# Performance work log

Measured on AMD Instinct MI355X. Metric: run time of the kernel, lower is better.

Reference implementation:

```python
import jax, jax.numpy as jnp
import numpy as np

D_MODEL = 1024
NUM_HEADS = 16
HEAD_DIM = D_MODEL // NUM_HEADS


def setup_inputs() -> dict:
    key = jax.random.key(0)
    ks = jax.random.split(key, 12)
    B, S, D = 4, 2048, D_MODEL
    s = 1.0 / np.sqrt(D)
    return {
        "query": jax.random.normal(ks[0], (B, S, D), jnp.float32),
        "key": jax.random.normal(ks[1], (B, S, D), jnp.float32),
        "value": jax.random.normal(ks[2], (B, S, D), jnp.float32),
        "Wq": jax.random.normal(ks[3], (D, D), jnp.float32) * s,
        "bq": jax.random.normal(ks[4], (D,), jnp.float32) * 0.02,
        "Wk": jax.random.normal(ks[5], (D, D), jnp.float32) * s,
        "bk": jax.random.normal(ks[6], (D,), jnp.float32) * 0.02,
        "Wv": jax.random.normal(ks[7], (D, D), jnp.float32) * s,
        "bv": jax.random.normal(ks[8], (D,), jnp.float32) * 0.02,
        "Wo": jax.random.normal(ks[9], (D, D), jnp.float32) * s,
        "bo": jax.random.normal(ks[10], (D,), jnp.float32) * 0.02,
    }


def _split_heads(x):
    B, S, D = x.shape
    return x.reshape(B, S, NUM_HEADS, HEAD_DIM).transpose(0, 2, 1, 3)  # [B,H,S,hd]


def reference(query, key, value, Wq, bq, Wk, bk, Wv, bv, Wo, bo):
    q = _split_heads(query @ Wq + bq)
    k = _split_heads(key @ Wk + bk)
    v = _split_heads(value @ Wv + bv)
    # NOTE: original scales by 1/sqrt(d_model), not 1/sqrt(head_dim)
    scale = 1.0 / np.sqrt(D_MODEL).astype(np.float32)
    scores = jnp.einsum('bhqd,bhkd->bhqk', q, k) * scale  # [B,H,S,S]
    attn = jax.nn.softmax(scores, axis=-1)
    out = jnp.einsum('bhqk,bhkd->bhqd', attn, v)  # [B,H,S,hd]
    B, H, S, hd = out.shape
    out = out.transpose(0, 2, 1, 3).reshape(B, S, D_MODEL)
    out = out @ Wo + bo
    return out, attn
```

## Files before the change

### kernel.cpp

```cpp
#include <hip/hip_runtime.h>
#include <hip/hip_bf16.h>

typedef __bf16 bf16;
typedef __bf16 bf16x8 __attribute__((ext_vector_type(8)));
typedef __bf16 bf16x4 __attribute__((ext_vector_type(4)));
typedef __bf16 bf16x2 __attribute__((ext_vector_type(2)));
typedef float  f32x4  __attribute__((ext_vector_type(4)));
typedef float  f32x16 __attribute__((ext_vector_type(16)));
typedef unsigned int u32;

#define MFMA(A, B, C)   __builtin_amdgcn_mfma_f32_16x16x32_bf16((A), (B), (C), 0, 0, 0)
#define MFMA32(A, B, C) __builtin_amdgcn_mfma_f32_32x32x16_bf16((A), (B), (C), 0, 0, 0)

static constexpr int BATCH = 4, S = 2048, D = 1024, NH = 16, HD = 64;
static constexpr int M = BATCH * S;
static constexpr float KL = 0.045084220027780106f;

__device__ __forceinline__ void gload16(const void* g, void* l) {
  __builtin_amdgcn_global_load_lds(
      (const __attribute__((address_space(1))) void*)g,
      (__attribute__((address_space(3))) void*)l, 16, 0, 0);
}

__device__ __forceinline__ float fexp2(float x) {
#if __has_builtin(__builtin_amdgcn_exp2f)
  return __builtin_amdgcn_exp2f(x);
#else
  return exp2f(x);
#endif
}

__device__ __forceinline__ u32 pack2(float a, float b) {
  union { bf16x2 h; u32 u; } c;
  c.h = (bf16x2){(bf16)a, (bf16)b};
  return c.u;
}

union U4 { u32 w[4]; bf16x8 v; };

#define WAITV_BAR(n)                                        \
  asm volatile("s_waitcnt vmcnt(" #n ")" ::: "memory");     \
  __builtin_amdgcn_s_barrier();                             \
  __builtin_amdgcn_sched_barrier(0);

__global__ __launch_bounds__(256) void wt_convert(
    const float* __restrict__ W0, const float* __restrict__ W1,
    const float* __restrict__ W2, const float* __restrict__ W3,
    bf16* __restrict__ WtAll)
{
  const float* W = blockIdx.y == 0 ? W0 : blockIdx.y == 1 ? W1
                 : blockIdx.y == 2 ? W2 : W3;
  bf16* dst = WtAll + (size_t)blockIdx.y * (D * D);
  int k0 = (blockIdx.x >> 4) * 64, n0 = (blockIdx.x & 15) * 64;
  __shared__ __align__(16) bf16 T[64][72];
  int tid = threadIdx.x;
#pragma unroll
  for (int i = 0; i < 4; ++i) {
    int c = tid + i * 256, r = c >> 4, seg = c & 15;
    float4 v = *reinterpret_cast<const float4*>(W + (size_t)(k0 + r) * D + n0 + seg * 4);
    T[seg * 4 + 0][r] = (bf16)v.x; T[seg * 4 + 1][r] = (bf16)v.y;
    T[seg * 4 + 2][r] = (bf16)v.z; T[seg * 4 + 3][r] = (bf16)v.w;
  }
  __syncthreads();
#pragma unroll
  for (int i = 0; i < 2; ++i) {
    int c = tid + i * 256, r = c >> 3, seg = c & 7;
    *reinterpret_cast<bf16x8*>(dst + (size_t)(n0 + r) * D + k0 + seg * 8) =
        *reinterpret_cast<const bf16x8*>(&T[r][seg * 8]);
  }
}

__global__ __launch_bounds__(256) void x_convert(
    const float* __restrict__ X0, const float* __restrict__ X1,
    const float* __restrict__ X2, bf16* __restrict__ Y)
{
  int t = blockIdx.y;
  const float* X = t == 0 ? X0 : t == 1 ? X1 : X2;
  bf16* Yp = Y + (size_t)t * M * D;
  int idx = blockIdx.x * 256 + threadIdx.x;
#pragma unroll
  for (int i = 0; i < 4; ++i) {
    size_t j = (size_t)idx + (size_t)i * 524288;
    float4 v = reinterpret_cast<const float4*>(X)[j];
    bf16x4 o; o[0] = (bf16)v.x; o[1] = (bf16)v.y; o[2] = (bf16)v.z; o[3] = (bf16)v.w;
    reinterpret_cast<bf16x4*>(Yp)[j] = o;
  }
}

__global__ __launch_bounds__(256) void qkv_gemm(
    const bf16* __restrict__ Xb, const bf16* __restrict__ WtAll,
    const float* __restrict__ bq, const float* __restrict__ bk, const float* __restrict__ bv,
    bf16* __restrict__ Qb, bf16* __restrict__ Kb, bf16* __restrict__ Vtb)
{
  int v = blockIdx.y;
  const bf16*  X    = Xb + (size_t)v * M * D;
  const bf16*  Wt   = WtAll + (size_t)v * (D * D);
  const float* bias = v == 0 ? bq : v == 1 ? bk : bv;

  int x = blockIdx.x;
  int swz = (x & 7) * 64 + (x >> 3);
  int mt = swz >> 3, nt = swz & 7;
  int m0 = mt * 128, n0 = nt * 128;
  int tid = threadIdx.x, lane = tid & 63, w = tid >> 6;
  int wm = (w >> 1) * 64, wn = (w & 1) * 64;
  int lr = lane & 15, lg = lane >> 4;

  __shared__ __align__(16) unsigned char smem[34816];
  auto As = reinterpret_cast<bf16(*)[128][32]>(smem);
  auto Bs = reinterpret_cast<bf16(*)[128][32]>(smem + 16384);

  f32x4 acc[4][4] = {};

  int srow = w * 32 + (lane >> 2);
  int scol = (lane & 3) * 8;

  auto stage = [&](int buf, int ks) {
    const bf16* ga = X + (size_t)(m0 + srow) * D + ks * 32 + scol;
    bf16* la = &As[buf][w * 32][0];
    gload16(ga, la);
    gload16(ga + 16 * D, la + 16 * 32);
    const bf16* gb = Wt + (size_t)(n0 + srow) * D + ks * 32 + scol;
    bf16* lb = &Bs[buf][w * 32][0];
    gload16(gb, lb);
    gload16(gb + 16 * D, lb + 16 * 32);
  };

  stage(0, 0);
  for (int ks = 0; ks < 32; ++ks) {
    __syncthreads();
    if (ks < 31) stage((ks + 1) & 1, ks + 1);
    int buf = ks & 1;
    bf16x8 af[4], bfr[4];
#pragma unroll
    for (int i = 0; i < 4; ++i)
      af[i] = *reinterpret_cast<const bf16x8*>(&As[buf][wm + i * 16 + lr][8 * lg]);
#pragma unroll
    for (int j = 0; j < 4; ++j)
      bfr[j] = *reinterpret_cast<const bf16x8*>(&Bs[buf][wn + j * 16 + lr][8 * lg]);
#pragma unroll
    for (int i = 0; i < 4; ++i)
#pragma unroll
      for (int j = 0; j < 4; ++j)
        acc[i][j] = MFMA(af[i], bfr[j], acc[i][j]);
  }
  __syncthreads();

  if (v < 2) {
    bf16* Out = v == 0 ? Qb : Kb;
    float qs = v == 0 ? KL : 1.0f;
    auto Es = reinterpret_cast<bf16(*)[128]>(smem);
#pragma unroll
    for (int i = 0; i < 4; ++i)
#pragma unroll
      for (int j = 0; j < 4; ++j) {
        int n = wn + j * 16 + lr;
        float bias_n = bias[n0 + n];
#pragma unroll
        for (int r = 0; r < 4; ++r)
          Es[wm + i * 16 + 4 * lg + r][n] = (bf16)((acc[i][j][r] + bias_n) * qs);
      }
    __syncthreads();
#pragma unroll
    for (int i = 0; i < 8; ++i) {
      int c = tid + i * 256, r = c >> 4, seg = c & 15;
      int mg = m0 + r, b = mg >> 11, s = mg & 2047;
      int ng = n0 + seg * 8, h = ng >> 6, d = ng & 63;
      *reinterpret_cast<bf16x8*>(Out + (((size_t)(b * NH + h)) * S + s) * HD + d) =
          *reinterpret_cast<const bf16x8*>(&Es[r][seg * 8]);
    }
  } else {
    auto Es = reinterpret_cast<bf16(*)[136]>(smem);
#pragma unroll
    for (int i = 0; i < 4; ++i)
#pragma unroll
      for (int j = 0; j < 4; ++j) {
        int n = wn + j * 16 + lr;
        float bias_n = bias[n0 + n];
        bf16x4 t;
#pragma unroll
        for (int r = 0; r < 4; ++r) t[r] = (bf16)(acc[i][j][r] + bias_n);
        *reinterpret_cast<bf16x4*>(&Es[n][wm + i * 16 + 4 * lg]) = t;
      }
    __syncthreads();
#pragma unroll
    for (int i = 0; i < 8; ++i) {
      int c = tid + i * 256, r = c >> 4, seg = c & 15;
      int ng = n0 + r, h = ng >> 6, d = ng & 63;
      int mg = m0 + seg * 8, b = mg >> 11, s = mg & 2047;
      *reinterpret_cast<bf16x8*>(Vtb + (((size_t)(b * NH + h)) * HD + d) * S + s) =
          *reinterpret_cast<const bf16x8*>(&Es[r][seg * 8]);
    }
  }
}

__global__ __launch_bounds__(256) void attn_kernel(
    const bf16* __restrict__ Qb, const bf16* __restrict__ Kb, const bf16* __restrict__ Vtb,
    float* __restrict__ attn_out, bf16* __restrict__ ctx)
{
  int xx = blockIdx.x;
  int xcd = xx & 7, r8 = xx >> 3;
  int bh = xcd + 8 * (r8 >> 5);
  int qb = r8 & 31;
  int tid = threadIdx.x, lane = tid & 63, w = tid >> 6;
  int q32 = lane & 31, hi = lane >> 5;
  int qh = w & 1, kh = w >> 1;

  __shared__ __align__(16) bf16 Ks[2][64][64];
  __shared__ __align__(16) bf16 Vs[2][64][64];
  __shared__ __align__(16) float Ps[64][68];
  __shared__ float sums[2][64];

  int q_row = qb * 64 + qh * 32 + q32;
  const bf16* Qrow = Qb + ((size_t)bh * S + q_row) * HD;
  bf16x8 qreg[4];
#pragma unroll
  for (int c = 0; c < 4; ++c)
    qreg[c] = *reinterpret_cast<const bf16x8*>(Qrow + c * 16 + 8 * hi);

  auto stageK = [&](int buf, int kc) {
    const bf16* base = Kb + ((size_t)bh * S + kc * 64) * HD;
#pragma unroll
    for (int i = 0; i < 2; ++i) {
      int c = i * 256 + tid, row = c >> 3, j = c & 7;
      gload16(base + row * HD + 8 * (j ^ (row & 7)),
              reinterpret_cast<bf16*>(&Ks[buf][0][0]) + c * 8);
    }
  };
  auto stageV = [&](int buf, int kc) {
    const bf16* base = Vtb + (size_t)bh * HD * S + kc * 64;
#pragma unroll
    for (int i = 0; i < 2; ++i) {
      int c = i * 256 + tid, row = c >> 3, j = c & 7;
      gload16(base + (size_t)row * S + 8 * (j ^ (row & 7)),
              reinterpret_cast<bf16*>(&Vs[buf][0][0]) + c * 8);
    }
  };

  int krow = kh * 32 + q32, ks7 = krow & 7;

  float lrun = 0.f;
  stageK(0, 0);
  for (int kc = 0; kc < 32; ++kc) {
    if (kc < 31) {
      stageK((kc + 1) & 1, kc + 1);
      WAITV_BAR(2)
    } else {
      WAITV_BAR(0)
    }
    int buf = kc & 1;
    f32x16 sa = {};
#pragma unroll
    for (int c = 0; c < 4; ++c) {
      bf16x8 kf = *reinterpret_cast<const bf16x8*>(&Ks[buf][krow][8 * ((2 * c + hi) ^ ks7)]);
      sa = MFMA32(kf, qreg[c], sa);
    }
#pragma unroll
    for (int r = 0; r < 16; ++r) lrun += fexp2(sa[r]);
    __builtin_amdgcn_s_barrier();
  }
  lrun += __shfl_xor(lrun, 32);
  if (hi == 0) sums[kh][qh * 32 + q32] = lrun;
  __syncthreads();
  float lg2l = __log2f(sums[0][qh * 32 + q32] + sums[1][qh * 32 + q32]);

  f32x16 oaccA = {}, oaccB = {};
  float* ablk = attn_out + ((size_t)bh * S + qb * 64) * S;

  auto computeB = [&](int buf) {
    f32x16 sa = {};
#pragma unroll
    for (int c = 0; c < 4; ++c) {
      bf16x8 kf = *reinterpret_cast<const bf16x8*>(&Ks[buf][krow][8 * ((2 * c + hi) ^ ks7)]);
      sa = MFMA32(kf, qreg[c], sa);
    }
    u32 pku[8];
#pragma unroll
    for (int rq = 0; rq < 4; ++rq) {
      f32x4 pv;
#pragma unroll
      for (int j = 0; j < 4; ++j) pv[j] = fexp2(sa[rq * 4 + j] - lg2l);
      *reinterpret_cast<f32x4*>(&Ps[qh * 32 + q32][kh * 32 + 8 * rq + 4 * hi]) = pv;
      pku[rq * 2 + 0] = pack2(pv[0], pv[1]);
      pku[rq * 2 + 1] = pack2(pv[2], pv[3]);
    }
#pragma unroll
    for (int c2 = 0; c2 < 2; ++c2) {
      u32 myw0 = hi ? pku[4 * c2 + 2] : pku[4 * c2 + 0];
      u32 myw1 = hi ? pku[4 * c2 + 3] : pku[4 * c2 + 1];
      u32 sdw0 = hi ? pku[4 * c2 + 0] : pku[4 * c2 + 2];
      u32 sdw1 = hi ? pku[4 * c2 + 1] : pku[4 * c2 + 3];
      u32 r0 = __shfl_xor(sdw0, 32);
      u32 r1 = __shfl_xor(sdw1, 32);
      U4 f;
      f.w[0] = hi ? r0 : myw0;
      f.w[1] = hi ? r1 : myw1;
      f.w[2] = hi ? myw0 : r0;
      f.w[3] = hi ? myw1 : r1;
      {
        int vrow = q32, vs7 = vrow & 7;
        bf16x8 vf = *reinterpret_cast<const bf16x8*>(
            &Vs[buf][vrow][8 * ((4 * kh + 2 * c2 + hi) ^ vs7)]);
        oaccA = MFMA32(f.v, vf, oaccA);
      }
      {
        int vrow = 32 + q32, vs7 = vrow & 7;
        bf16x8 vf = *reinterpret_cast<const bf16x8*>(
            &Vs[buf][vrow][8 * ((4 * kh + 2 * c2 + hi) ^ vs7)]);
        oaccB = MFMA32(f.v, vf, oaccB);
      }
    }
  };

  int prow = tid >> 2, pc0 = (tid & 3) * 4;
  auto storeP = [&](int kc) {
    float* dst = ablk + (size_t)prow * S + kc * 64 + pc0;
#pragma unroll
    for (int i = 0; i < 4; ++i)
      __builtin_nontemporal_store(
          *reinterpret_cast<const f32x4*>(&Ps[prow][pc0 + 16 * i]),
          reinterpret_cast<f32x4*>(dst + 16 * i));
  };

  stageK(0, 0); stageV(0, 0);
  stageK(1, 1); stageV(1, 1);
  WAITV_BAR(4)
  computeB(0);
  __builtin_amdgcn_s_barrier();
  storeP(0);

  for (int kc = 1; kc < 32; ++kc) {
    if (kc < 31) {
      stageK((kc + 1) & 1, kc + 1);
      stageV((kc + 1) & 1, kc + 1);
      WAITV_BAR(8)
    } else {
      WAITV_BAR(4)
    }
    computeB(kc & 1);
    __builtin_amdgcn_s_barrier();
    storeP(kc);
  }

  float* fbuf = reinterpret_cast<float*>(&Ks[0][0][0]);
  if (kh == 1) {
#pragma unroll
    for (int reg = 0; reg < 16; ++reg) {
      int qloc = (reg & 3) + 8 * (reg >> 2) + 4 * hi;
      fbuf[(qh * 32 + qloc) * 64 + q32]      = oaccA[reg];
      fbuf[(qh * 32 + qloc) * 64 + 32 + q32] = oaccB[reg];
    }
  }
  __syncthreads();
  bf16* cs = reinterpret_cast<bf16*>(&Vs[0][0][0]);
  if (kh == 0) {
#pragma unroll
    for (int reg = 0; reg < 16; ++reg) {
      int qloc = (reg & 3) + 8 * (reg >> 2) + 4 * hi;
      cs[(qh * 32 + qloc) * 72 + q32] =
          (bf16)(oaccA[reg] + fbuf[(qh * 32 + qloc) * 64 + q32]);
      cs[(qh * 32 + qloc) * 72 + 32 + q32] =
          (bf16)(oaccB[reg] + fbuf[(qh * 32 + qloc) * 64 + 32 + q32]);
    }
  }
  __syncthreads();
  {
    int b = bh >> 4, h = bh & 15;
    int row = tid >> 2, cseg = (tid & 3) * 16;
    bf16* cp = ctx + ((size_t)b * S + qb * 64 + row) * D + h * HD + cseg;
    *reinterpret_cast<bf16x8*>(cp) =
        *reinterpret_cast<const bf16x8*>(&cs[row * 72 + cseg]);
    *reinterpret_cast<bf16x8*>(cp + 8) =
        *reinterpret_cast<const bf16x8*>(&cs[row * 72 + cseg + 8]);
  }
}

__global__ __launch_bounds__(256) void out_gemm(
    const bf16* __restrict__ ctx, const bf16* __restrict__ Wto,
    const float* __restrict__ bo, float* __restrict__ Out)
{
  int x = blockIdx.x;
  int swz = (x & 7) * 64 + (x >> 3);
  int mt = swz >> 3, nt = swz & 7;
  int m0 = mt * 128, n0 = nt * 128;
  int tid = threadIdx.x, lane = tid & 63, w = tid >> 6;
  int wm = (w >> 1) * 64, wn = (w & 1) * 64;
  int lr = lane & 15, lg = lane >> 4;

  __shared__ __align__(16) bf16 As[2][128][32];
  __shared__ __align__(16) bf16 Bs[2][128][32];

  f32x4 acc[4][4] = {};

  int srow = w * 32 + (lane >> 2);
  int scol = (lane & 3) * 8;

  auto stage = [&](int buf, int ks) {
    const bf16* ga = ctx + (size_t)(m0 + srow) * D + ks * 32 + scol;
    bf16* la = &As[buf][w * 32][0];
    gload16(ga, la);
    gload16(ga + 16 * D, la + 16 * 32);
    const bf16* gb = Wto + (size_t)(n0 + srow) * D + ks * 32 + scol;
    bf16* lb = &Bs[buf][w * 32][0];
    gload16(gb, lb);
    gload16(gb + 16 * D, lb + 16 * 32);
  };

  stage(0, 0);
  for (int ks = 0; ks < 32; ++ks) {
    __syncthreads();
    if (ks < 31) stage((ks + 1) & 1, ks + 1);
    int buf = ks & 1;
    bf16x8 af[4], bfr[4];
#pragma unroll
    for (int i = 0; i < 4; ++i)
      af[i] = *reinterpret_cast<const bf16x8*>(&As[buf][wm + i * 16 + lr][8 * lg]);
#pragma unroll
    for (int j = 0; j < 4; ++j)
      bfr[j] = *reinterpret_cast<const bf16x8*>(&Bs[buf][wn + j * 16 + lr][8 * lg]);
#pragma unroll
    for (int i = 0; i < 4; ++i)
#pragma unroll
      for (int j = 0; j < 4; ++j)
        acc[i][j] = MFMA(af[i], bfr[j], acc[i][j]);
  }

#pragma unroll
  for (int i = 0; i < 4; ++i)
#pragma unroll
    for (int j = 0; j < 4; ++j) {
      int n = n0 + wn + j * 16 + lr;
      float bias_n = bo[n];
#pragma unroll
      for (int r = 0; r < 4; ++r)
        Out[(size_t)(m0 + wm + i * 16 + 4 * lg + r) * D + n] = acc[i][j][r] + bias_n;
    }
}

extern "C" void kernel_launch(void* const* d_in, const int* in_sizes, int n_in,
                              void* d_out, int out_size, void* d_ws, size_t ws_size,
                              hipStream_t stream)
{
  const float* query = (const float*)d_in[0];
  const float* key   = (const float*)d_in[1];
  const float* value = (const float*)d_in[2];
  const float* Wq = (const float*)d_in[3]; const float* bq = (const float*)d_in[4];
  const float* Wk = (const float*)d_in[5]; const float* bk = (const float*)d_in[6];
  const float* Wv = (const float*)d_in[7]; const float* bv = (const float*)d_in[8];
  const float* Wo = (const float*)d_in[9]; const float* bo = (const float*)d_in[10];

  float* out  = (float*)d_out;
  float* attn = out + (size_t)M * D;

  char* ws = (char*)d_ws;
  const size_t MiB = 1048576;
  bf16* WtAll = (bf16*)ws;
  bf16* Xb    = (bf16*)(ws + 8 * MiB);
  bf16* Qb    = (bf16*)(ws + 56 * MiB);
  bf16* Kb    = (bf16*)(ws + 72 * MiB);
  bf16* Vtb   = (bf16*)(ws + 88 * MiB);
  bf16* ctx   = Xb;

  wt_convert<<<dim3(256, 4), 256, 0, stream>>>(Wq, Wk, Wv, Wo, WtAll);
  x_convert<<<dim3(2048, 3), 256, 0, stream>>>(query, key, value, Xb);
  qkv_gemm<<<dim3(512, 3), 256, 0, stream>>>(Xb, WtAll, bq, bk, bv, Qb, Kb, Vtb);
  attn_kernel<<<dim3(2048), 256, 0, stream>>>(Qb, Kb, Vtb, attn, ctx);
  out_gemm<<<dim3(512), 256, 0, stream>>>(ctx, WtAll + (size_t)3 * D * D, bo, out);
}
```

Baseline: 442.4 us.

## Merge conversion kernels, split exp-sum accumulators, add LDS fences to barriers

Combines the weight-transpose and activation-conversion kernels into one launch, which removes a kernel launch and its tail. The attention row-sum pass now spreads its exp accumulation over four partial sums to shorten the dependency chain. Barriers also wait for lgkmcnt(0) before syncing, and a __syncthreads is added before the output reduction, which fixes an LDS ordering hazard. These extra waits can cost a little latency inside the attention loop.

```diff
diff --git a/kernel.cpp b/kernel.cpp
--- a/kernel.cpp
+++ b/kernel.cpp
@@ -38,52 +38,60 @@
 
 union U4 { u32 w[4]; bf16x8 v; };
 
-#define WAITV_BAR(n)                                        \
-  asm volatile("s_waitcnt vmcnt(" #n ")" ::: "memory");     \
-  __builtin_amdgcn_s_barrier();                             \
+#define WAITV_BAR(n)                                                     \
+  asm volatile("s_waitcnt vmcnt(" #n ") lgkmcnt(0)" ::: "memory");       \
+  __builtin_amdgcn_s_barrier();                                          \
   __builtin_amdgcn_sched_barrier(0);
 
-__global__ __launch_bounds__(256) void wt_convert(
+#define FENCE_BAR                                                        \
+  asm volatile("s_waitcnt lgkmcnt(0)" ::: "memory");                     \
+  __builtin_amdgcn_s_barrier();                                          \
+  __builtin_amdgcn_sched_barrier(0);
+
+__global__ __launch_bounds__(256) void convert_all(
+    const float* __restrict__ X0, const float* __restrict__ X1,
+    const float* __restrict__ X2,
     const float* __restrict__ W0, const float* __restrict__ W1,
     const float* __restrict__ W2, const float* __restrict__ W3,
-    bf16* __restrict__ WtAll)
+    bf16* __restrict__ Xb, bf16* __restrict__ WtAll)
 {
-  const float* W = blockIdx.y == 0 ? W0 : blockIdx.y == 1 ? W1
-                 : blockIdx.y == 2 ? W2 : W3;
-  bf16* dst = WtAll + (size_t)blockIdx.y * (D * D);
-  int k0 = (blockIdx.x >> 4) * 64, n0 = (blockIdx.x & 15) * 64;
-  __shared__ __align__(16) bf16 T[64][72];
+  int blk = blockIdx.x;
   int tid = threadIdx.x;
-#pragma unroll
-  for (int i = 0; i < 4; ++i) {
-    int c = tid + i * 256, r = c >> 4, seg = c & 15;
-    float4 v = *reinterpret_cast<const float4*>(W + (size_t)(k0 + r) * D + n0 + seg * 4);
-    T[seg * 4 + 0][r] = (bf16)v.x; T[seg * 4 + 1][r] = (bf16)v.y;
-    T[seg * 4 + 2][r] = (bf16)v.z; T[seg * 4 + 3][r] = (bf16)v.w;
-  }
-  __syncthreads();
-#pragma unroll
-  for (int i = 0; i < 2; ++i) {
-    int c = tid + i * 256, r = c >> 3, seg = c & 7;
-    *reinterpret_cast<bf16x8*>(dst + (size_t)(n0 + r) * D + k0 + seg * 8) =
-        *reinterpret_cast<const bf16x8*>(&T[r][seg * 8]);
-  }
-}
-
-__global__ __launch_bounds__(256) void x_convert(
-    const float* __restrict__ X0, const float* __restrict__ X1,
-    const float* __restrict__ X2, bf16* __restrict__ Y)
-{
-  int t = blockIdx.y;
-  const float* X = t == 0 ? X0 : t == 1 ? X1 : X2;
-  bf16* Yp = Y + (size_t)t * M * D;
-  int idx = blockIdx.x * 256 + threadIdx.x;
-#pragma unroll
-  for (int i = 0; i < 4; ++i) {
-    size_t j = (size_t)idx + (size_t)i * 524288;
-    float4 v = reinterpret_cast<const float4*>(X)[j];
-    bf16x4 o; o[0] = (bf16)v.x; o[1] = (bf16)v.y; o[2] = (bf16)v.z; o[3] = (bf16)v.w;
-    reinterpret_cast<bf16x4*>(Yp)[j] = o;
+  if (blk < 6144) {
+    int t = blk >> 11;
+    int bx = blk & 2047;
+    const float* X = t == 0 ? X0 : t == 1 ? X1 : X2;
+    bf16* Yp = Xb + (size_t)t * M * D;
+    int idx = bx * 256 + tid;
+#pragma unroll
+    for (int i = 0; i < 4; ++i) {
+      size_t j = (size_t)idx + (size_t)i * 524288;
+      float4 v = reinterpret_cast<const float4*>(X)[j];
+      bf16x4 o; o[0] = (bf16)v.x; o[1] = (bf16)v.y; o[2] = (bf16)v.z; o[3] = (bf16)v.w;
+      reinterpret_cast<bf16x4*>(Yp)[j] = o;
+    }
+  } else {
+    int wb = blk - 6144;
+    int wy = wb >> 8;
+    int bx = wb & 255;
+    const float* W = wy == 0 ? W0 : wy == 1 ? W1 : wy == 2 ? W2 : W3;
+    bf16* dst = WtAll + (size_t)wy * (D * D);
+    int k0 = (bx >> 4) * 64, n0 = (bx & 15) * 64;
+    __shared__ __align__(16) bf16 T[64][72];
+#pragma unroll
+    for (int i = 0; i < 4; ++i) {
+      int c = tid + i * 256, r = c >> 4, seg = c & 15;
+      float4 v = *reinterpret_cast<const float4*>(W + (size_t)(k0 + r) * D + n0 + seg * 4);
+      T[seg * 4 + 0][r] = (bf16)v.x; T[seg * 4 + 1][r] = (bf16)v.y;
+      T[seg * 4 + 2][r] = (bf16)v.z; T[seg * 4 + 3][r] = (bf16)v.w;
+    }
+    __syncthreads();
+#pragma unroll
+    for (int i = 0; i < 2; ++i) {
+      int c = tid + i * 256, r = c >> 3, seg = c & 7;
+      *reinterpret_cast<bf16x8*>(dst + (size_t)(n0 + r) * D + k0 + seg * 8) =
+          *reinterpret_cast<const bf16x8*>(&T[r][seg * 8]);
+    }
   }
 }
 
@@ -238,7 +246,7 @@
 
   int krow = kh * 32 + q32, ks7 = krow & 7;
 
-  float lrun = 0.f;
+  float xs[4] = {0.f, 0.f, 0.f, 0.f};
   stageK(0, 0);
   for (int kc = 0; kc < 32; ++kc) {
     if (kc < 31) {
@@ -255,9 +263,10 @@
       sa = MFMA32(kf, qreg[c], sa);
     }
 #pragma unroll
-    for (int r = 0; r < 16; ++r) lrun += fexp2(sa[r]);
-    __builtin_amdgcn_s_barrier();
-  }
+    for (int r = 0; r < 16; ++r) xs[r & 3] += fexp2(sa[r]);
+    FENCE_BAR
+  }
+  float lrun = (xs[0] + xs[1]) + (xs[2] + xs[3]);
   lrun += __shfl_xor(lrun, 32);
   if (hi == 0) sums[kh][qh * 32 + q32] = lrun;
   __syncthreads();
@@ -325,7 +334,7 @@
   stageK(1, 1); stageV(1, 1);
   WAITV_BAR(4)
   computeB(0);
-  __builtin_amdgcn_s_barrier();
+  FENCE_BAR
   storeP(0);
 
   for (int kc = 1; kc < 32; ++kc) {
@@ -337,11 +346,12 @@
       WAITV_BAR(4)
     }
     computeB(kc & 1);
-    __builtin_amdgcn_s_barrier();
+    FENCE_BAR
     storeP(kc);
   }
 
   float* fbuf = reinterpret_cast<float*>(&Ks[0][0][0]);
+  __syncthreads();
   if (kh == 1) {
 #pragma unroll
     for (int reg = 0; reg < 16; ++reg) {
@@ -460,8 +470,8 @@
   bf16* Vtb   = (bf16*)(ws + 88 * MiB);
   bf16* ctx   = Xb;
 
-  wt_convert<<<dim3(256, 4), 256, 0, stream>>>(Wq, Wk, Wv, Wo, WtAll);
-  x_convert<<<dim3(2048, 3), 256, 0, stream>>>(query, key, value, Xb);
+  convert_all<<<dim3(7168), 256, 0, stream>>>(query, key, value,
+                                              Wq, Wk, Wv, Wo, Xb, WtAll);
   qkv_gemm<<<dim3(512, 3), 256, 0, stream>>>(Xb, WtAll, bq, bk, bv, Qb, Kb, Vtb);
   attn_kernel<<<dim3(2048), 256, 0, stream>>>(Qb, Kb, Vtb, attn, ctx);
   out_gemm<<<dim3(512), 256, 0, stream>>>(ctx, WtAll + (size_t)3 * D * D, bo, out);
```

After: 440.2 us. Within noise of the previous version (-0.5%).
